# Performance work log

Measured on AMD Instinct MI355X. Metric: run time of the kernel, lower is better.

## Reference

```python
import jax, jax.numpy as jnp
import numpy as np

BETA = 1.0

def setup_inputs() -> dict:
    key = jax.random.key(0)
    k1, k2, k3 = jax.random.split(key, 3)
    B, T, G, D, V = 4, 2048, 8, 128, 1024
    inputs = jax.random.normal(k1, (B, T, G * D), dtype=jnp.float32)
    paddings = jax.random.randint(k2, (B, T), 0, 2, dtype=jnp.int32)
    codebook = jax.random.normal(k3, (V, G, D), dtype=jnp.float32)  # (V, G, D)
    return {"inputs": inputs, "paddings": paddings, "codebook": codebook}

def reference(inputs, paddings, codebook):
    B, T, _ = inputs.shape
    V, G, D = codebook.shape
    sg = jax.lax.stop_gradient
    x = inputs.reshape(B, T, G, D)
    x2 = jnp.sum(x * x, axis=-1)                      # (B,T,G)
    c2 = jnp.sum(codebook * codebook, axis=-1)        # (V,G)
    xc = jnp.einsum('btgd,vgd->btvg', x, codebook)    # (B,T,V,G) GEMM
    dist = x2[:, :, None, :] - 2.0 * xc + c2[None, None]
    ids = jnp.argmin(dist, axis=2)                    # (B,T,G) int
    # gather codebook[ids[b,t,g], g] -> (B,T,G,D)
    quantized = codebook[ids, jnp.arange(G)[None, None, :]]
    mask = (1 - paddings).astype(jnp.float32)[:, :, None, None]  # (B,T,1,1)
    msum = mask.sum()
    kmeans_loss = jnp.sum(((quantized - sg(x)) ** 2) * mask) / msum
    commitment_loss = jnp.sum(((x - sg(quantized)) ** 2) * mask) / msum
    total_loss = kmeans_loss + BETA * commitment_loss
    quantized_st = ((x + sg(quantized - x)) * mask).reshape(B, T, G * D)
    ids = jnp.where((paddings == 1)[:, :, None], -1, ids.astype(jnp.int32))
    return (ids, quantized_st, kmeans_loss, commitment_loss, total_loss)
```

## Files before the change

kernel.cpp:

```cpp
#include <hip/hip_runtime.h>
#include <math.h>

typedef _Float16 f16;
typedef f16 half8 __attribute__((ext_vector_type(8)));
typedef float f32x4 __attribute__((ext_vector_type(4)));

#define BT 8192
#define NG 8
#define ND 128
#define NV 1024
#define MARGIN  0.08f
#define MARGIN3 0.16f
#define BM 64
#define BN 64
#define NT 16
#define FULLBIT 0x40000000u

#define OUT_IDS 0
#define OUT_Q   65536
#define OUT_L   (65536 + 8388608)

#define OFF_C2A   0
#define OFF_C2B   8192
#define OFF_LOSSG 81920
#define OFF_CNT   147456
#define OFF_FLAGS 147464
#define OFF_CBH   213000
#define OFF_PART  (OFF_CBH + 524288)
#define OFF_CAND2 (OFF_PART + 64)

__device__ __forceinline__ void gll16(const f16* g, f16* l) {
    __builtin_amdgcn_global_load_lds(
        (const __attribute__((address_space(1))) unsigned int*)g,
        (__attribute__((address_space(3))) unsigned int*)l, 16, 0, 0);
}

__global__ __launch_bounds__(256) void prep_kernel(
    const float* __restrict__ cb, f16* __restrict__ cbh,
    float* __restrict__ c2a, float* __restrict__ c2b, int* __restrict__ cnt) {
    __shared__ float prod[16][16][9];
    __shared__ float rbuf[16][8];
    const int tid = threadIdx.x;
    const int rloc = tid >> 4, t = tid & 15;
    const int idx = blockIdx.x * 16 + rloc;
    if (blockIdx.x == 0 && tid == 0) *cnt = 0;
    const int v = idx >> 3, g = idx & 7;
    const int rl = v & 63;
    const float4* row4 = (const float4*)(cb + (size_t)idx * ND);

    float4 a = row4[t * 2], b = row4[t * 2 + 1];
    float vv[8] = {a.x, a.y, a.z, a.w, b.x, b.y, b.z, b.w};
    half8 h;
#pragma unroll
    for (int e = 0; e < 8; ++e) {
        prod[rloc][t][e] = __fmul_rn(vv[e], vv[e]);
        h[e] = (f16)vv[e];
    }
    int cn = v >> 6;
    size_t base = ((size_t)(g * 16 + cn)) * 8192 + rl * 128;
    *(half8*)(cbh + base + ((t ^ (rl & 7)) * 8)) = h;
    __syncthreads();

    if (t < 8) {
        float r = 0.f;
#pragma unroll
        for (int tt = 0; tt < 16; ++tt)
            r = __fadd_rn(r, prod[rloc][tt][t]);
        rbuf[rloc][t] = r;
    }
    __syncthreads();
    if (t == 0) {
        float s = __fadd_rn(
            __fadd_rn(__fadd_rn(rbuf[rloc][0], rbuf[rloc][1]),
                      __fadd_rn(rbuf[rloc][2], rbuf[rloc][3])),
            __fadd_rn(__fadd_rn(rbuf[rloc][4], rbuf[rloc][5]),
                      __fadd_rn(rbuf[rloc][6], rbuf[rloc][7])));
        c2a[idx] = s;
        c2b[g * NV + v] = s;
    }
}

__global__ __launch_bounds__(256, 4) void mfma_gemm(
    const float* __restrict__ x, const f16* __restrict__ cbh,
    const float* __restrict__ cb, const float* __restrict__ c2b,
    const int* __restrict__ pad, float* __restrict__ out_ids,
    float* __restrict__ out_q, float* __restrict__ lossg,
    int* __restrict__ cnt, int* __restrict__ flags,
    int* __restrict__ cand2) {
    __shared__ __align__(16) f16 Bh[2][BN * ND];
    __shared__ __align__(16) float c2s[NV];
    __shared__ int idsL[BM];

    const int tid = threadIdx.x;
    const int b = blockIdx.x;
    const int g = b & 7;
    const int tok0 = (b >> 3) * BM;
    const int lane = tid & 63;
    const int w = tid >> 6;
    const int wr = w & 1, wc = w >> 1;
    const int l15 = lane & 15, l4 = lane >> 4;

    ((float4*)c2s)[tid] = ((const float4*)(c2b + (size_t)g * NV))[tid];
    {
        const f16* sh = cbh + ((size_t)(g * 16 + 0)) * 8192;
#pragma unroll
        for (int it = 0; it < 4; ++it)
            gll16(sh + it * 2048 + tid * 8, &Bh[0][it * 2048 + tid * 8]);
    }

    half8 ah[4][2];
#pragma unroll
    for (int kk = 0; kk < 4; ++kk)
#pragma unroll
        for (int ti = 0; ti < 2; ++ti) {
            const float* ap = x + ((size_t)(tok0 + wr * 32 + ti * 16 + l15) * NG + g) * ND
                              + kk * 32 + l4 * 8;
            float4 p0 = *(const float4*)ap, p1 = *(const float4*)(ap + 4);
            float vv[8] = {p0.x, p0.y, p0.z, p0.w, p1.x, p1.y, p1.z, p1.w};
            half8 h;
#pragma unroll
            for (int j = 0; j < 8; ++j) h[j] = (f16)vv[j];
            ah[kk][ti] = h;
        }

    float d1s[2][4], d2s[2][4], d3s[2][4];
    int id1s[2][4], id2s[2][4];
#pragma unroll
    for (int ti = 0; ti < 2; ++ti)
#pragma unroll
        for (int r = 0; r < 4; ++r) {
            d1s[ti][r] = INFINITY;
            d2s[ti][r] = INFINITY;
            d3s[ti][r] = INFINITY;
            id1s[ti][r] = 0;
            id2s[ti][r] = 0;
        }

    int buf = 0;
#pragma unroll 1
    for (int t = 0; t < NT; ++t) {
        asm volatile("s_waitcnt vmcnt(0) lgkmcnt(0)" ::: "memory");
        __builtin_amdgcn_s_barrier();
        __builtin_amdgcn_sched_barrier(0);

        if (t + 1 < NT) {
            const f16* sh = cbh + ((size_t)(g * 16 + t + 1)) * 8192;
#pragma unroll
            for (int it = 0; it < 4; ++it)
                gll16(sh + it * 2048 + tid * 8,
                      &Bh[buf ^ 1][it * 2048 + tid * 8]);
        }

        f32x4 acc[2][2];
#pragma unroll
        for (int ti = 0; ti < 2; ++ti)
#pragma unroll
            for (int tj = 0; tj < 2; ++tj)
                acc[ti][tj] = (f32x4){0.f, 0.f, 0.f, 0.f};

#pragma unroll
        for (int kk = 0; kk < 4; ++kk) {
            half8 bh[2];
#pragma unroll
            for (int tj = 0; tj < 2; ++tj) {
                int rw = wc * 32 + tj * 16 + l15;
                bh[tj] = *(const half8*)(
                    &Bh[buf][rw * 128 + (((kk * 4 + l4) ^ (rw & 7)) << 3)]);
            }
#pragma unroll
            for (int ti = 0; ti < 2; ++ti)
#pragma unroll
                for (int tj = 0; tj < 2; ++tj)
                    acc[ti][tj] = __builtin_amdgcn_mfma_f32_16x16x32_f16(
                        ah[kk][ti], bh[tj], acc[ti][tj], 0, 0, 0);
        }

#pragma unroll
        for (int tj = 0; tj < 2; ++tj) {
            int code = t * BN + wc * 32 + tj * 16 + l15;
            float c2v = c2s[code];
#pragma unroll
            for (int ti = 0; ti < 2; ++ti)
#pragma unroll
                for (int r = 0; r < 4; ++r) {
                    float dv = fmaf(-2.0f, acc[ti][tj][r], c2v);
                    bool lt1 = dv < d1s[ti][r];
                    bool lt2 = dv < d2s[ti][r];
                    bool lt3 = dv < d3s[ti][r];
                    d3s[ti][r] = lt2 ? d2s[ti][r] : (lt3 ? dv : d3s[ti][r]);
                    d2s[ti][r] = lt1 ? d1s[ti][r] : (lt2 ? dv : d2s[ti][r]);
                    id2s[ti][r] = lt1 ? id1s[ti][r] : (lt2 ? code : id2s[ti][r]);
                    d1s[ti][r] = lt1 ? dv : d1s[ti][r];
                    id1s[ti][r] = lt1 ? code : id1s[ti][r];
                }
        }
        buf ^= 1;
    }

    __syncthreads();
    float4* red = (float4*)&Bh[0][0];
    float* redd3 = (float*)(red + 128);
#pragma unroll
    for (int ti = 0; ti < 2; ++ti)
#pragma unroll
        for (int r = 0; r < 4; ++r) {
            float d1 = d1s[ti][r], d2 = d2s[ti][r], d3 = d3s[ti][r];
            int i1 = id1s[ti][r], i2 = id2s[ti][r];
#pragma unroll
            for (int m = 1; m < 16; m <<= 1) {
                float od1 = __shfl_xor(d1, m);
                float od2 = __shfl_xor(d2, m);
                float od3 = __shfl_xor(d3, m);
                int oi1 = __shfl_xor(i1, m);
                int oi2 = __shfl_xor(i2, m);
                bool ow = od1 < d1;
                float w1 = ow ? od1 : d1, w2 = ow ? od2 : d2, w3 = ow ? od3 : d3;
                int wi1 = ow ? oi1 : i1, wi2 = ow ? oi2 : i2;
                float l1 = ow ? d1 : od1, l2 = ow ? d2 : od2;
                int li1 = ow ? i1 : oi1;
                d1 = w1; i1 = wi1;
                bool t2 = w2 < l1;
                d2 = t2 ? w2 : l1;
                i2 = t2 ? wi2 : li1;
                d3 = t2 ? fminf(w3, l1) : fminf(w2, l2);
            }
            if (l15 == 0) {
                int o = wc * BM + wr * 32 + ti * 16 + l4 * 4 + r;
                red[o] = make_float4(d1, __int_as_float(i1), d2,
                                     __int_as_float(i2));
                redd3[o] = d3;
            }
        }
    __syncthreads();

    if (tid < BM) {
        float4 A = red[tid], C = red[BM + tid];
        float a3 = redd3[tid], c3 = redd3[BM + tid];
        float a1 = A.x, a2 = A.z, c1 = C.x, c2q = C.z;
        int ai1 = __float_as_int(A.y), ai2 = __float_as_int(A.w);
        int ci1 = __float_as_int(C.y), ci2 = __float_as_int(C.w);
        bool cw = c1 < a1;
        float w1 = cw ? c1 : a1, w2 = cw ? c2q : a2, w3 = cw ? c3 : a3;
        int wi1 = cw ? ci1 : ai1, wi2 = cw ? ci2 : ai2;
        float l1 = cw ? a1 : c1, l2 = cw ? a2 : c2q;
        int li1 = cw ? ai1 : ci1;
        float d1 = w1;
        int i1 = wi1;
        bool t2 = w2 < l1;
        float d2 = t2 ? w2 : l1;
        int i2 = t2 ? wi2 : li1;
        float d3 = t2 ? fminf(w3, l1) : fminf(w2, l2);

        int tok = tok0 + tid;
        int idx = tok * NG + g;
        int p = pad[tok];
        out_ids[idx] = p ? -1.0f : (float)i1;
        idsL[tid] = p ? -1 : i1;
        if (!p && d2 - d1 < MARGIN) {
            int pos = atomicAdd(cnt, 1);
            flags[pos] = idx;
            cand2[idx] = i2 | ((d3 - d1 < MARGIN3) ? (int)FULLBIT : 0);
        }
    }
    __syncthreads();

#pragma unroll
    for (int it = 0; it < 8; ++it) {
        int i = it * 256 + tid;
        int tl = i >> 5, d4 = i & 31;
        int id = idsL[tl];
        float4 q = make_float4(0.f, 0.f, 0.f, 0.f);
        float s = 0.f;
        size_t rowo = ((size_t)(tok0 + tl) * NG + g) * ND;
        if (id >= 0) {
            q = ((const float4*)(cb + ((size_t)id * NG + g) * ND))[d4];
            float4 a = ((const float4*)(x + rowo))[d4];
            float e0 = q.x - a.x, e1 = q.y - a.y;
            float e2 = q.z - a.z, e3 = q.w - a.w;
            s = e0 * e0 + e1 * e1 + e2 * e2 + e3 * e3;
        }
        ((float4*)(out_q + rowo))[d4] = q;
#pragma unroll
        for (int m = 1; m < 32; m <<= 1) s += __shfl_xor(s, m);
        if (d4 == 0) lossg[(tok0 + tl) * NG + g] = (id >= 0) ? s : 0.0f;
    }
}

__global__ __launch_bounds__(256) void recheck(
    const float* __restrict__ x, const int* __restrict__ pad,
    const float* __restrict__ cb, const float* __restrict__ c2w,
    const int* __restrict__ cnt, const int* __restrict__ flags,
    const int* __restrict__ cand2, float* __restrict__ out_ids,
    float* __restrict__ out_q, float* __restrict__ lossg) {
    __shared__ __align__(16) float xs[ND];
    __shared__ float2 redw[4];
    __shared__ int bidS;
    const int tid = threadIdx.x;
    const int lane = tid & 63;
    const int w = tid >> 6;
    const int n_f = cnt[0];

    for (int f = blockIdx.x * 4 + w; f < n_f; f += gridDim.x * 4) {
        int idx = flags[f];
        unsigned cc = (unsigned)cand2[idx];
        if (cc & FULLBIT) continue;
        int g = idx & 7;
        int id1 = (int)out_ids[idx];
        int id2 = (int)(cc & ~FULLBIT);
        float2 xv = ((const float2*)(x + (size_t)idx * ND))[lane];
        float2 av = ((const float2*)(cb + ((size_t)id1 * NG + g) * ND))[lane];
        float2 bv = ((const float2*)(cb + ((size_t)id2 * NG + g) * ND))[lane];
        float eA0 = xv.x - av.x, eA1 = xv.y - av.y;
        float eB0 = xv.x - bv.x, eB1 = xv.y - bv.y;
        float sA = eA0 * eA0 + eA1 * eA1;
        float sB = eB0 * eB0 + eB1 * eB1;
#pragma unroll
        for (int m = 1; m < 64; m <<= 1) {
            sA += __shfl_xor(sA, m);
            sB += __shfl_xor(sB, m);
        }
        int win;
        float sw;
        if (sA < sB) { win = id1; sw = sA; }
        else if (sB < sA) { win = id2; sw = sB; }
        else { win = (id1 < id2) ? id1 : id2; sw = sA; }
        if (win != id1) {
            if (lane == 0) {
                out_ids[idx] = (float)win;
                lossg[idx] = sw;
            }
            if (lane < 32) {
                float4 q = ((const float4*)(cb + ((size_t)win * NG + g) * ND))[lane];
                ((float4*)(out_q + (size_t)idx * ND))[lane] = q;
            }
        }
    }
    __syncthreads();

    for (int f = blockIdx.x; f < n_f; f += gridDim.x) {
        int idx = flags[f];
        if (!(((unsigned)cand2[idx]) & FULLBIT)) continue;
        int g = idx & 7;
        __syncthreads();
        if (tid < 32)
            ((float4*)xs)[tid] = ((const float4*)(x + (size_t)idx * ND))[tid];
        __syncthreads();

        float rr[8];
#pragma unroll
        for (int j = 0; j < 8; ++j) rr[j] = 0.0f;
#pragma unroll
        for (int i = 0; i < 32; ++i) {
            float4 v = ((const float4*)xs)[i];
            int j0 = (i * 4) & 7;
            rr[j0 + 0] = __fadd_rn(rr[j0 + 0], __fmul_rn(v.x, v.x));
            rr[j0 + 1] = __fadd_rn(rr[j0 + 1], __fmul_rn(v.y, v.y));
            rr[j0 + 2] = __fadd_rn(rr[j0 + 2], __fmul_rn(v.z, v.z));
            rr[j0 + 3] = __fadd_rn(rr[j0 + 3], __fmul_rn(v.w, v.w));
        }
        float x2v = __fadd_rn(
            __fadd_rn(__fadd_rn(rr[0], rr[1]), __fadd_rn(rr[2], rr[3])),
            __fadd_rn(__fadd_rn(rr[4], rr[5]), __fadd_rn(rr[6], rr[7])));

        float best = INFINITY;
        int bid = 0x7FFFFFFF;
        float s0 = 0.f, s1 = 0.f, s2 = 0.f, s3 = 0.f;
#pragma unroll
        for (int i = 0; i < 32; ++i) {
            float4 a = ((const float4*)xs)[i];
            float4 q0 = ((const float4*)(cb + ((size_t)(tid) * NG + g) * ND))[i];
            float4 q1 = ((const float4*)(cb + ((size_t)(tid + 256) * NG + g) * ND))[i];
            float4 q2 = ((const float4*)(cb + ((size_t)(tid + 512) * NG + g) * ND))[i];
            float4 q3 = ((const float4*)(cb + ((size_t)(tid + 768) * NG + g) * ND))[i];
            s0 = fmaf(a.x, q0.x, s0); s0 = fmaf(a.y, q0.y, s0);
            s0 = fmaf(a.z, q0.z, s0); s0 = fmaf(a.w, q0.w, s0);
            s1 = fmaf(a.x, q1.x, s1); s1 = fmaf(a.y, q1.y, s1);
            s1 = fmaf(a.z, q1.z, s1); s1 = fmaf(a.w, q1.w, s1);
            s2 = fmaf(a.x, q2.x, s2); s2 = fmaf(a.y, q2.y, s2);
            s2 = fmaf(a.z, q2.z, s2); s2 = fmaf(a.w, q2.w, s2);
            s3 = fmaf(a.x, q3.x, s3); s3 = fmaf(a.y, q3.y, s3);
            s3 = fmaf(a.z, q3.z, s3); s3 = fmaf(a.w, q3.w, s3);
        }
        float dd[4] = {s0, s1, s2, s3};
#pragma unroll
        for (int jj = 0; jj < 4; ++jj) {
            int c = tid + 256 * jj;
            float d = __fadd_rn(__fsub_rn(x2v, __fmul_rn(2.0f, dd[jj])),
                                c2w[(size_t)c * NG + g]);
            if (d < best || (d == best && c < bid)) { best = d; bid = c; }
        }
#pragma unroll
        for (int m = 1; m < 64; m <<= 1) {
            float od = __shfl_xor(best, m);
            int ob = __shfl_xor(bid, m);
            if (od < best || (od == best && ob < bid)) { best = od; bid = ob; }
        }
        if (lane == 0) redw[w] = make_float2(best, __int_as_float(bid));
        __syncthreads();
        if (tid == 0) {
            float b2 = redw[0].x;
            int i2 = __float_as_int(redw[0].y);
#pragma unroll
            for (int ww = 1; ww < 4; ++ww) {
                float ob = redw[ww].x;
                int oi = __float_as_int(redw[ww].y);
                if (ob < b2 || (ob == b2 && oi < i2)) { b2 = ob; i2 = oi; }
            }
            out_ids[idx] = (float)i2;
            bidS = i2;
        }
        __syncthreads();
        if (tid < 32) {
            float4 q = ((const float4*)(cb + ((size_t)bidS * NG + g) * ND))[tid];
            ((float4*)(out_q + (size_t)idx * ND))[tid] = q;
            float4 a = ((const float4*)xs)[tid];
            float e0 = q.x - a.x, e1 = q.y - a.y;
            float e2 = q.z - a.z, e3 = q.w - a.w;
            float s = e0 * e0 + e1 * e1 + e2 * e2 + e3 * e3;
#pragma unroll
            for (int m = 1; m < 32; m <<= 1) s += __shfl_xor(s, m);
            if (tid == 0) lossg[idx] = s;
        }
    }
}

__global__ __launch_bounds__(256) void loss_part(
    const float* __restrict__ lossg, float* __restrict__ part) {
    __shared__ float sr[256];
    const int tid = threadIdx.x;
    float4 v = ((const float4*)lossg)[blockIdx.x * 256 + tid];
    sr[tid] = ((v.x + v.y) + (v.z + v.w));
    __syncthreads();
    for (int st = 128; st > 0; st >>= 1) {
        if (tid < st) sr[tid] += sr[tid + st];
        __syncthreads();
    }
    if (tid == 0) part[blockIdx.x] = sr[0];
}

__global__ __launch_bounds__(256) void final_kernel(
    const int* __restrict__ pad, const float* __restrict__ part,
    float* __restrict__ out_l) {
    __shared__ int mr[256];
    const int tid = threadIdx.x;
    int m = 0;
#pragma unroll
    for (int i = 0; i < 32; ++i) m += 1 - pad[tid * 32 + i];
    mr[tid] = m;
    __syncthreads();
    for (int st = 128; st > 0; st >>= 1) {
        if (tid < st) mr[tid] += mr[tid + st];
        __syncthreads();
    }
    if (tid == 0) {
        float s = 0.f;
#pragma unroll
        for (int i = 0; i < 64; ++i) s += part[i];
        float k = s / (float)mr[0];
        out_l[0] = k;
        out_l[1] = k;
        out_l[2] = k + k;
    }
}

extern "C" void kernel_launch(void* const* d_in, const int* in_sizes, int n_in,
                              void* d_out, int out_size, void* d_ws, size_t ws_size,
                              hipStream_t stream) {
    const float* x = (const float*)d_in[0];
    const int* pad = (const int*)d_in[1];
    const float* cb = (const float*)d_in[2];
    float* out = (float*)d_out;
    float* ws = (float*)d_ws;

    float* ws_c2a = ws + OFF_C2A;
    float* ws_c2b = ws + OFF_C2B;
    float* ws_lossg = ws + OFF_LOSSG;
    int* ws_cnt = (int*)(ws + OFF_CNT);
    int* ws_flags = (int*)(ws + OFF_FLAGS);
    f16* cbh = (f16*)(ws + OFF_CBH);
    float* ws_part = ws + OFF_PART;
    int* ws_cand2 = (int*)(ws + OFF_CAND2);

    prep_kernel<<<NV * NG / 16, 256, 0, stream>>>(cb, cbh, ws_c2a, ws_c2b,
                                                  ws_cnt);
    mfma_gemm<<<(BT / BM) * NG, 256, 0, stream>>>(x, cbh, cb, ws_c2b, pad,
                                                  out + OUT_IDS, out + OUT_Q,
                                                  ws_lossg, ws_cnt, ws_flags,
                                                  ws_cand2);
    recheck<<<512, 256, 0, stream>>>(x, pad, cb, ws_c2a, ws_cnt, ws_flags,
                                     ws_cand2, out + OUT_IDS, out + OUT_Q,
                                     ws_lossg);
    loss_part<<<64, 256, 0, stream>>>(ws_lossg, ws_part);
    final_kernel<<<1, 256, 0, stream>>>(pad, ws_part, out + OUT_L);
}
```

Baseline: 89.38 us.

## Compact non-padded tokens and skip GEMM work for padded tokens

Builds a compacted list of non-padded token indices in the prep kernel using an atomic counter. The GEMM/argmin kernel then processes only those tokens in tiles and exits early for tiles beyond the count. A new padfill kernel writes -1 ids, zero outputs and zero loss for padded tokens. This roughly halves GEMM work at the cost of gathered, non-contiguous x loads and scattered output writes, an extra launch and a memset; the order of tokmap entries is nondeterministic.

```diff
diff --git a/kernel.cpp b/kernel.cpp
--- a/kernel.cpp
+++ b/kernel.cpp
@@ -20,14 +20,15 @@
 #define OUT_Q   65536
 #define OUT_L   (65536 + 8388608)
 
-#define OFF_C2A   0
-#define OFF_C2B   8192
-#define OFF_LOSSG 81920
-#define OFF_CNT   147456
-#define OFF_FLAGS 147464
-#define OFF_CBH   213000
-#define OFF_PART  (OFF_CBH + 524288)
-#define OFF_CAND2 (OFF_PART + 64)
+#define OFF_C2A    0
+#define OFF_C2B    8192
+#define OFF_LOSSG  81920
+#define OFF_CNT    147456
+#define OFF_FLAGS  147464
+#define OFF_CBH    213000
+#define OFF_PART   (OFF_CBH + 524288)
+#define OFF_CAND2  (OFF_PART + 64)
+#define OFF_TOKMAP (OFF_CAND2 + 65536)
 
 __device__ __forceinline__ void gll16(const f16* g, f16* l) {
     __builtin_amdgcn_global_load_lds(
@@ -36,17 +37,25 @@
 }
 
 __global__ __launch_bounds__(256) void prep_kernel(
-    const float* __restrict__ cb, f16* __restrict__ cbh,
-    float* __restrict__ c2a, float* __restrict__ c2b, int* __restrict__ cnt) {
+    const float* __restrict__ cb, const int* __restrict__ pad,
+    f16* __restrict__ cbh, float* __restrict__ c2a, float* __restrict__ c2b,
+    int* __restrict__ ncnt, int* __restrict__ tokmap) {
     __shared__ float prod[16][16][9];
     __shared__ float rbuf[16][8];
     const int tid = threadIdx.x;
     const int rloc = tid >> 4, t = tid & 15;
     const int idx = blockIdx.x * 16 + rloc;
-    if (blockIdx.x == 0 && tid == 0) *cnt = 0;
     const int v = idx >> 3, g = idx & 7;
     const int rl = v & 63;
     const float4* row4 = (const float4*)(cb + (size_t)idx * ND);
+
+    if (tid < 16) {
+        int tok = blockIdx.x * 16 + tid;
+        if (!pad[tok]) {
+            int p = atomicAdd(ncnt, 1);
+            tokmap[p] = tok;
+        }
+    }
 
     float4 a = row4[t * 2], b = row4[t * 2 + 1];
     float vv[8] = {a.x, a.y, a.z, a.w, b.x, b.y, b.z, b.w};
@@ -80,21 +89,38 @@
     }
 }
 
+__global__ __launch_bounds__(256) void padfill(
+    const int* __restrict__ pad, float* __restrict__ out_ids,
+    float* __restrict__ out_q, float* __restrict__ lossg) {
+    const int tok = blockIdx.x;
+    if (!pad[tok]) return;
+    const int tid = threadIdx.x;
+    ((float4*)(out_q + (size_t)tok * (NG * ND)))[tid] =
+        make_float4(0.f, 0.f, 0.f, 0.f);
+    if (tid < NG) {
+        out_ids[tok * NG + tid] = -1.0f;
+        lossg[tok * NG + tid] = 0.0f;
+    }
+}
+
 __global__ __launch_bounds__(256, 4) void mfma_gemm(
     const float* __restrict__ x, const f16* __restrict__ cbh,
     const float* __restrict__ cb, const float* __restrict__ c2b,
-    const int* __restrict__ pad, float* __restrict__ out_ids,
-    float* __restrict__ out_q, float* __restrict__ lossg,
-    int* __restrict__ cnt, int* __restrict__ flags,
-    int* __restrict__ cand2) {
+    const int* __restrict__ ncnt, const int* __restrict__ tokmap,
+    float* __restrict__ out_ids, float* __restrict__ out_q,
+    float* __restrict__ lossg, int* __restrict__ cnt,
+    int* __restrict__ flags, int* __restrict__ cand2) {
     __shared__ __align__(16) f16 Bh[2][BN * ND];
     __shared__ __align__(16) float c2s[NV];
     __shared__ int idsL[BM];
+    __shared__ int tokL[BM];
 
     const int tid = threadIdx.x;
     const int b = blockIdx.x;
     const int g = b & 7;
-    const int tok0 = (b >> 3) * BM;
+    const int count = *ncnt;
+    const int tile_base = (b >> 3) * BM;
+    if (tile_base >= count) return;
     const int lane = tid & 63;
     const int w = tid >> 6;
     const int wr = w & 1, wc = w >> 1;
@@ -108,12 +134,19 @@
             gll16(sh + it * 2048 + tid * 8, &Bh[0][it * 2048 + tid * 8]);
     }
 
+    int tokA_[2];
+#pragma unroll
+    for (int ti = 0; ti < 2; ++ti) {
+        int slot = tile_base + wr * 32 + ti * 16 + l15;
+        tokA_[ti] = tokmap[(slot < count) ? slot : 0];
+    }
+
     half8 ah[4][2];
 #pragma unroll
     for (int kk = 0; kk < 4; ++kk)
 #pragma unroll
         for (int ti = 0; ti < 2; ++ti) {
-            const float* ap = x + ((size_t)(tok0 + wr * 32 + ti * 16 + l15) * NG + g) * ND
+            const float* ap = x + ((size_t)tokA_[ti] * NG + g) * ND
                               + kk * 32 + l4 * 8;
             float4 p0 = *(const float4*)ap, p1 = *(const float4*)(ap + 4);
             float vv[8] = {p0.x, p0.y, p0.z, p0.w, p1.x, p1.y, p1.z, p1.w};
@@ -251,15 +284,20 @@
         int i2 = t2 ? wi2 : li1;
         float d3 = t2 ? fminf(w3, l1) : fminf(w2, l2);
 
-        int tok = tok0 + tid;
-        int idx = tok * NG + g;
-        int p = pad[tok];
-        out_ids[idx] = p ? -1.0f : (float)i1;
-        idsL[tid] = p ? -1 : i1;
-        if (!p && d2 - d1 < MARGIN) {
-            int pos = atomicAdd(cnt, 1);
-            flags[pos] = idx;
-            cand2[idx] = i2 | ((d3 - d1 < MARGIN3) ? (int)FULLBIT : 0);
+        int slot = tile_base + tid;
+        if (slot < count) {
+            int tok = tokmap[slot];
+            int idx = tok * NG + g;
+            out_ids[idx] = (float)i1;
+            idsL[tid] = i1;
+            tokL[tid] = tok;
+            if (d2 - d1 < MARGIN) {
+                int pos = atomicAdd(cnt, 1);
+                flags[pos] = idx;
+                cand2[idx] = i2 | ((d3 - d1 < MARGIN3) ? (int)FULLBIT : 0);
+            }
+        } else {
+            idsL[tid] = -1;
         }
     }
     __syncthreads();
@@ -269,29 +307,28 @@
         int i = it * 256 + tid;
         int tl = i >> 5, d4 = i & 31;
         int id = idsL[tl];
-        float4 q = make_float4(0.f, 0.f, 0.f, 0.f);
-        float s = 0.f;
-        size_t rowo = ((size_t)(tok0 + tl) * NG + g) * ND;
         if (id >= 0) {
-            q = ((const float4*)(cb + ((size_t)id * NG + g) * ND))[d4];
+            int tok = tokL[tl];
+            size_t rowo = ((size_t)tok * NG + g) * ND;
+            float4 q = ((const float4*)(cb + ((size_t)id * NG + g) * ND))[d4];
             float4 a = ((const float4*)(x + rowo))[d4];
             float e0 = q.x - a.x, e1 = q.y - a.y;
             float e2 = q.z - a.z, e3 = q.w - a.w;
-            s = e0 * e0 + e1 * e1 + e2 * e2 + e3 * e3;
-        }
-        ((float4*)(out_q + rowo))[d4] = q;
-#pragma unroll
-        for (int m = 1; m < 32; m <<= 1) s += __shfl_xor(s, m);
-        if (d4 == 0) lossg[(tok0 + tl) * NG + g] = (id >= 0) ? s : 0.0f;
+            float s = e0 * e0 + e1 * e1 + e2 * e2 + e3 * e3;
+            ((float4*)(out_q + rowo))[d4] = q;
+#pragma unroll
+            for (int m = 1; m < 32; m <<= 1) s += __shfl_xor(s, m);
+            if (d4 == 0) lossg[tok * NG + g] = s;
+        }
     }
 }
 
 __global__ __launch_bounds__(256) void recheck(
-    const float* __restrict__ x, const int* __restrict__ pad,
-    const float* __restrict__ cb, const float* __restrict__ c2w,
-    const int* __restrict__ cnt, const int* __restrict__ flags,
-    const int* __restrict__ cand2, float* __restrict__ out_ids,
-    float* __restrict__ out_q, float* __restrict__ lossg) {
+    const float* __restrict__ x, const float* __restrict__ cb,
+    const float* __restrict__ c2w, const int* __restrict__ cnt,
+    const int* __restrict__ flags, const int* __restrict__ cand2,
+    float* __restrict__ out_ids, float* __restrict__ out_q,
+    float* __restrict__ lossg) {
     __shared__ __align__(16) float xs[ND];
     __shared__ float2 redw[4];
     __shared__ int bidS;
@@ -480,14 +517,19 @@
     f16* cbh = (f16*)(ws + OFF_CBH);
     float* ws_part = ws + OFF_PART;
     int* ws_cand2 = (int*)(ws + OFF_CAND2);
-
-    prep_kernel<<<NV * NG / 16, 256, 0, stream>>>(cb, cbh, ws_c2a, ws_c2b,
-                                                  ws_cnt);
-    mfma_gemm<<<(BT / BM) * NG, 256, 0, stream>>>(x, cbh, cb, ws_c2b, pad,
+    int* ws_tokmap = (int*)(ws + OFF_TOKMAP);
+
+    hipMemsetAsync(ws_cnt, 0, 8, stream);
+    prep_kernel<<<NV * NG / 16, 256, 0, stream>>>(cb, pad, cbh, ws_c2a,
+                                                  ws_c2b, ws_cnt + 1,
+                                                  ws_tokmap);
+    padfill<<<BT, 256, 0, stream>>>(pad, out + OUT_IDS, out + OUT_Q, ws_lossg);
+    mfma_gemm<<<(BT / BM) * NG, 256, 0, stream>>>(x, cbh, cb, ws_c2b,
+                                                  ws_cnt + 1, ws_tokmap,
                                                   out + OUT_IDS, out + OUT_Q,
                                                   ws_lossg, ws_cnt, ws_flags,
                                                   ws_cand2);
-    recheck<<<512, 256, 0, stream>>>(x, pad, cb, ws_c2a, ws_cnt, ws_flags,
+    recheck<<<512, 256, 0, stream>>>(x, cb, ws_c2a, ws_cnt, ws_flags,
                                      ws_cand2, out + OUT_IDS, out + OUT_Q,
                                      ws_lossg);
     loss_part<<<64, 256, 0, stream>>>(ws_lossg, ws_part);
```

Measured after the change: 85.08 us. -4.8%, faster.
